# Kernel optimization log

Measured on AMD Instinct MI355X. Metric: run time of the kernel, lower is better.

## Reference

```python
import jax, jax.numpy as jnp
import numpy as np

K_MASK = -2.3819763e+38
NUM_HEADS = 16
NUM_KV_HEADS = 8
HEAD_DIM = 128
FEATURES = 2048
QUERY_SCALE = 0.08838834764831845  # head_dim ** -0.5
ROPE_BASE = 10000
SOFT_CAP = 50.0
WINDOW = 1024


def apply_rope(inputs, positions, base_frequency=ROPE_BASE):
    # inputs: [B, L, N, H], positions: [B, L]
    head_dim = inputs.shape[-1]
    fraction = 2.0 * jnp.arange(0, head_dim // 2, dtype=jnp.float32) / head_dim
    timescale = jnp.asarray(base_frequency, jnp.float32) ** fraction
    sinusoid = positions[..., None].astype(jnp.float32) / timescale[None, None, :]
    sinusoid = sinusoid[..., None, :]  # [B, L, 1, H/2]
    sin, cos = jnp.sin(sinusoid), jnp.cos(sinusoid)
    first, second = jnp.split(inputs, 2, axis=-1)
    out = jnp.concatenate([first * cos - second * sin,
                           second * cos + first * sin], axis=-1)
    return out.astype(inputs.dtype)


def setup_inputs() -> dict:
    key = jax.random.key(0)
    ks = jax.random.split(key, 4)
    B, T, D = 2, 2048, FEATURES
    x = jax.random.normal(ks[0], (B, T, D), dtype=jnp.float32)
    segment_pos = jnp.broadcast_to(jnp.arange(T, dtype=jnp.int32)[None, :], (B, T))
    # causal prefill mask [B, T, S] with S == T
    attn_mask = jnp.broadcast_to(
        jnp.tril(jnp.ones((T, T), dtype=bool))[None], (B, T, T))
    wq = jax.random.normal(ks[1], (NUM_HEADS, D, HEAD_DIM), dtype=jnp.float32) * 0.02
    wkv = jax.random.normal(ks[2], (2, NUM_KV_HEADS, D, HEAD_DIM), dtype=jnp.float32) * 0.02
    wo = jax.random.normal(ks[3], (NUM_HEADS, HEAD_DIM, D), dtype=jnp.float32) * 0.02
    return {"x": x, "segment_pos": segment_pos, "attn_mask": attn_mask,
            "wq": wq, "wkv": wkv, "wo": wo}


def reference(x, segment_pos, attn_mask, wq, wkv, wo):
    # Projections
    q = jnp.einsum('BTD,NDH->BTNH', x, wq)              # [B,T,N,H]
    kv = jnp.einsum('BSD,CKDH->CBSKH', x, wkv)          # [2,B,S,K,H]
    k, v = kv[0], kv[1]

    # RoPE + query scaling
    q = apply_rope(q, segment_pos) * QUERY_SCALE
    k = apply_rope(k, segment_pos)

    # GQA: fold query heads into (K groups, G heads per group)
    B, T, N, H = q.shape
    K, G = NUM_KV_HEADS, N // NUM_KV_HEADS
    qg = q.reshape(B, T, K, G, H)
    logits = jnp.einsum('BTKGH,BSKH->BTKGS', qg, k).reshape(B, T, N, -1)

    # Logit soft-capping
    logits = jnp.tanh(logits / SOFT_CAP) * SOFT_CAP

    # Sliding-window mask (prefill: end_index=0, cache_len = S)
    S = attn_mask.shape[-1]
    cache_positions = jnp.arange(S)[None, None, :]       # [1,1,S]
    sp = segment_pos[:, :, None]                         # [B,T,1]
    sliding = (cache_positions > sp - WINDOW) & (cache_positions < sp + WINDOW)
    mask = jnp.logical_and(attn_mask, sliding)

    padded = jnp.where(mask[:, :, None, :], logits, K_MASK)
    probs = jax.nn.softmax(padded, axis=-1).astype(k.dtype)

    pg = probs.reshape(B, T, K, G, S)
    encoded = jnp.einsum('BTKGS,BSKH->BTKGH', pg, v).reshape(B, T, N, H)
    return jnp.einsum('BTNH,NHD->BTD', encoded, wo)
```

## Files before the change

kernel.cpp:

```cpp
#include <hip/hip_runtime.h>

typedef __attribute__((ext_vector_type(8))) short short8;
typedef __attribute__((ext_vector_type(4))) float f32x4;
typedef __attribute__((ext_vector_type(4))) float f4;
typedef __attribute__((ext_vector_type(4))) unsigned short u16x4;

#define MFMA_B16 __builtin_amdgcn_mfma_f32_16x16x32_bf16

__device__ __forceinline__ unsigned short f2bf(float f) {
    union { float f; unsigned int u; } v; v.f = f;
    unsigned int r = v.u + 0x7fffu + ((v.u >> 16) & 1u);
    return (unsigned short)(r >> 16);
}
__device__ __forceinline__ float bf2f(unsigned short h) {
    union { unsigned int u; float f; } v; v.u = ((unsigned int)h) << 16;
    return v.f;
}
__device__ __forceinline__ float fexp2(float x) {
    float r; asm("v_exp_f32 %0, %1" : "=v"(r) : "v"(x)); return r;
}
__device__ __forceinline__ unsigned int cvt_pk_bf16(float lo, float hi) {
    unsigned int r;
    asm("v_cvt_pk_bf16_f32 %0, %1, %2" : "=v"(r) : "v"(lo), "v"(hi));
    return r;
}
__device__ __forceinline__ void gload_lds16(const void* g, void* l) {
    __builtin_amdgcn_global_load_lds(
        (const __attribute__((address_space(1))) unsigned int*)g,
        (__attribute__((address_space(3))) unsigned int*)l, 16, 0, 0);
}


__global__ void conv_x(const float* __restrict__ x, unsigned short* __restrict__ xb) {
    int i = blockIdx.x * 256 + threadIdx.x;
    f4 v = ((const f4*)x)[i];
    u16x4 o;
    o[0] = f2bf(v[0]); o[1] = f2bf(v[1]); o[2] = f2bf(v[2]); o[3] = f2bf(v[3]);
    ((u16x4*)xb)[i] = o;
}

__global__ void conv_wqkvt(const float* __restrict__ wq, const float* __restrict__ wkv,
                           unsigned short* __restrict__ wt) {
    __shared__ float tile[64 * 65];
    const int d0 = blockIdx.x * 64, f0 = blockIdx.y * 64;
    const int head = f0 >> 7;
    const int h0 = f0 & 127;
    const float* src;
    float scl;
    if (head < 16)      { src = wq + (size_t)head * 2048 * 128;         scl = 0.08838834764831845f; }
    else if (head < 24) { src = wkv + (size_t)(head - 16) * 2048 * 128; scl = 0.057707801635558534f; }
    else                { src = wkv + (size_t)(head - 16) * 2048 * 128; scl = 1.f; }
    {
        int hh = threadIdx.x & 63, dq = threadIdx.x >> 6;
        #pragma unroll
        for (int r = 0; r < 16; ++r) {
            int dd = r * 4 + dq;
            tile[dd * 65 + hh] = src[(size_t)(d0 + dd) * 128 + h0 + hh] * scl;
        }
    }
    __syncthreads();
    {
        int dd = threadIdx.x & 63, fq = threadIdx.x >> 6;
        #pragma unroll
        for (int r = 0; r < 16; ++r) {
            int fl = r * 4 + fq;
            wt[(size_t)(f0 + fl) * 2048 + d0 + dd] = f2bf(tile[dd * 65 + fl]);
        }
    }
}

__global__ void conv_wot(const float* __restrict__ wo, unsigned short* __restrict__ wt) {
    __shared__ float tile[64 * 65];
    const int d0 = blockIdx.x * 64, r0 = blockIdx.y * 64;
    int cc = threadIdx.x & 63, rq = threadIdx.x >> 6;
    #pragma unroll
    for (int r = 0; r < 16; ++r) {
        int rr = r * 4 + rq;
        tile[rr * 65 + cc] = wo[(size_t)(r0 + rr) * 2048 + d0 + cc];
    }
    __syncthreads();
    #pragma unroll
    for (int r = 0; r < 16; ++r) {
        int rr = r * 4 + rq;
        wt[(size_t)(d0 + rr) * 2048 + r0 + cc] = f2bf(tile[cc * 65 + rr]);
    }
}


__global__ __launch_bounds__(512, 2)
void gemm8p(const unsigned short* __restrict__ A,
            const unsigned short* __restrict__ Bt,
            unsigned short* __restrict__ C,
            int ldk, int ldc, int nt, int ksplit, size_t cstride) {
    __shared__ __align__(16) unsigned short LDS[65536];
    const int tid = threadIdx.x, lane = tid & 63, w = tid >> 6;
    const int wr = w >> 2, wc = w & 3;
    const int l15 = lane & 15, l4 = lane >> 4;
    int nwg = gridDim.x * gridDim.y;
    int wg = blockIdx.y * gridDim.x + blockIdx.x;
    int swz = (wg & 7) * (nwg >> 3) + (wg >> 3);
    int bx = swz % gridDim.x, by = swz / gridDim.x;
    int slice = 0;
    if (ksplit) { slice = by & 1; by >>= 1; }
    unsigned short* Cs = C + (size_t)slice * cstride;
    const int brow = by * 256, bcol = bx * 256;
    const size_t koff = (size_t)slice * nt * 64;
    const int wg_a = w & 3;
    const int wg_b = wr;
    const int rA = wg_a * 8 + (lane >> 3);
    const int rB = wg_b * 8 + (lane >> 3);
    const int cgS = ((lane & 7) ^ (lane >> 3)) * 8;
    const unsigned short* aP = A + (size_t)(brow + wr * 128 + rA) * ldk + koff + cgS;
    const unsigned short* bP = Bt + (size_t)(bcol + wc * 64 + rB) * ldk + koff + cgS;
    const int ldsA0 = wr * 8192 + (wg_a * 64 + lane) * 8;
    const int ldsB0 = wc * 4096 + (wg_b * 64 + lane) * 8;
    const int aRd = (wr * 128 + l15) * 64;
    const int bRd = (wc * 64 + l15) * 64;
    const int c0 = ((0 + l4) ^ (l15 & 7)) * 8;
    const int c1 = ((4 + l4) ^ (l15 & 7)) * 8;
    f32x4 acc[8][4] = {};
    gload_lds16(aP,                    &LDS[ldsA0]);
    gload_lds16(bP,                    &LDS[16384 + ldsB0]);
    gload_lds16(aP + (size_t)32 * ldk, &LDS[ldsA0 + 2048]);
    gload_lds16(bP + (size_t)16 * ldk, &LDS[16384 + ldsB0 + 1024]);
    gload_lds16(bP + (size_t)32 * ldk, &LDS[16384 + ldsB0 + 2048]);
    gload_lds16(bP + (size_t)48 * ldk, &LDS[16384 + ldsB0 + 3072]);
    gload_lds16(aP + (size_t)64 * ldk, &LDS[ldsA0 + 4096]);
    gload_lds16(aP + (size_t)96 * ldk, &LDS[ldsA0 + 6144]);
    {
        const unsigned short* a1 = aP + 64;
        const unsigned short* b1 = bP + 64;
        gload_lds16(a1,                    &LDS[32768 + ldsA0]);
        gload_lds16(b1,                    &LDS[49152 + ldsB0]);
        gload_lds16(a1 + (size_t)32 * ldk, &LDS[32768 + ldsA0 + 2048]);
        gload_lds16(b1 + (size_t)16 * ldk, &LDS[49152 + ldsB0 + 1024]);
        gload_lds16(b1 + (size_t)32 * ldk, &LDS[49152 + ldsB0 + 2048]);
        gload_lds16(b1 + (size_t)48 * ldk, &LDS[49152 + ldsB0 + 3072]);
    }
    asm volatile("s_waitcnt vmcnt(6)" ::: "memory");
    __builtin_amdgcn_s_barrier();
    __builtin_amdgcn_sched_barrier(0);

    short8 af[4][2], bl[2][2], bh[2][2];
    for (int t = 0; t < nt - 1; ++t) {
        const int bufA = (t & 1) << 15, bufB = bufA + 16384;
        const int sA = ((t + 1) & 1) << 15;
        const bool pf2 = (t + 2) < nt;
        const unsigned short* ap1 = aP + (size_t)(t + 1) * 64;
        const unsigned short* ap2 = aP + (size_t)(t + 2) * 64;
        const unsigned short* bp2 = bP + (size_t)(t + 2) * 64;
        #pragma unroll
        for (int m = 0; m < 4; ++m) {
            af[m][0] = *(const short8*)&LDS[bufA + aRd + m * 1024 + c0];
            af[m][1] = *(const short8*)&LDS[bufA + aRd + m * 1024 + c1];
        }
        #pragma unroll
        for (int n = 0; n < 2; ++n) {
            bl[n][0] = *(const short8*)&LDS[bufB + bRd + n * 1024 + c0];
            bl[n][1] = *(const short8*)&LDS[bufB + bRd + n * 1024 + c1];
        }
        gload_lds16(ap1 + (size_t)64 * ldk, &LDS[sA + ldsA0 + 4096]);
        gload_lds16(ap1 + (size_t)96 * ldk, &LDS[sA + ldsA0 + 6144]);
        __builtin_amdgcn_s_barrier();
        __builtin_amdgcn_sched_barrier(0);
        __builtin_amdgcn_s_setprio(1);
        #pragma unroll
        for (int kk = 0; kk < 2; ++kk)
            #pragma unroll
            for (int m = 0; m < 4; ++m)
                #pragma unroll
                for (int n = 0; n < 2; ++n)
                    acc[m][n] = MFMA_B16(af[m][kk], bl[n][kk], acc[m][n], 0, 0, 0);
        __builtin_amdgcn_s_setprio(0);
        asm volatile("s_waitcnt vmcnt(6)" ::: "memory");
        __builtin_amdgcn_s_barrier();
        __builtin_amdgcn_sched_barrier(0);
        #pragma unroll
        for (int n = 0; n < 2; ++n) {
            bh[n][0] = *(const short8*)&LDS[bufB + bRd + (n + 2) * 1024 + c0];
            bh[n][1] = *(const short8*)&LDS[bufB + bRd + (n + 2) * 1024 + c1];
        }
        if (pf2) { gload_lds16(ap2, &LDS[bufA + ldsA0]);
                   gload_lds16(bp2, &LDS[bufB + ldsB0]); }
        __builtin_amdgcn_s_barrier();
        __builtin_amdgcn_sched_barrier(0);
        __builtin_amdgcn_s_setprio(1);
        #pragma unroll
        for (int kk = 0; kk < 2; ++kk)
            #pragma unroll
            for (int m = 0; m < 4; ++m)
                #pragma unroll
                for (int n = 0; n < 2; ++n)
                    acc[m][n + 2] = MFMA_B16(af[m][kk], bh[n][kk], acc[m][n + 2], 0, 0, 0);
        __builtin_amdgcn_s_setprio(0);
        asm volatile("s_waitcnt vmcnt(6)" ::: "memory");
        __builtin_amdgcn_s_barrier();
        __builtin_amdgcn_sched_barrier(0);
        #pragma unroll
        for (int m = 0; m < 4; ++m) {
            af[m][0] = *(const short8*)&LDS[bufA + aRd + (m + 4) * 1024 + c0];
            af[m][1] = *(const short8*)&LDS[bufA + aRd + (m + 4) * 1024 + c1];
        }
        if (pf2) { gload_lds16(ap2 + (size_t)32 * ldk, &LDS[bufA + ldsA0 + 2048]);
                   gload_lds16(bp2 + (size_t)16 * ldk, &LDS[bufB + ldsB0 + 1024]); }
        __builtin_amdgcn_s_barrier();
        __builtin_amdgcn_sched_barrier(0);
        __builtin_amdgcn_s_setprio(1);
        #pragma unroll
        for (int kk = 0; kk < 2; ++kk)
            #pragma unroll
            for (int m = 0; m < 4; ++m)
                #pragma unroll
                for (int n = 0; n < 2; ++n)
                    acc[m + 4][n] = MFMA_B16(af[m][kk], bl[n][kk], acc[m + 4][n], 0, 0, 0);
        __builtin_amdgcn_s_setprio(0);
        asm volatile("s_waitcnt vmcnt(6)" ::: "memory");
        __builtin_amdgcn_s_barrier();
        __builtin_amdgcn_sched_barrier(0);
        if (pf2) { gload_lds16(bp2 + (size_t)32 * ldk, &LDS[bufB + ldsB0 + 2048]);
                   gload_lds16(bp2 + (size_t)48 * ldk, &LDS[bufB + ldsB0 + 3072]); }
        __builtin_amdgcn_s_barrier();
        __builtin_amdgcn_sched_barrier(0);
        __builtin_amdgcn_s_setprio(1);
        #pragma unroll
        for (int kk = 0; kk < 2; ++kk)
            #pragma unroll
            for (int m = 0; m < 4; ++m)
                #pragma unroll
                for (int n = 0; n < 2; ++n)
                    acc[m + 4][n + 2] = MFMA_B16(af[m][kk], bh[n][kk], acc[m + 4][n + 2], 0, 0, 0);
        __builtin_amdgcn_s_setprio(0);
        asm volatile("s_waitcnt vmcnt(6)" ::: "memory");
        __builtin_amdgcn_s_barrier();
        __builtin_amdgcn_sched_barrier(0);
    }
    asm volatile("s_waitcnt vmcnt(0)" ::: "memory");
    __builtin_amdgcn_s_barrier();
    {
        const int bufA = ((nt - 1) & 1) << 15, bufB = bufA + 16384;
        #pragma unroll
        for (int m = 0; m < 4; ++m) {
            af[m][0] = *(const short8*)&LDS[bufA + aRd + m * 1024 + c0];
            af[m][1] = *(const short8*)&LDS[bufA + aRd + m * 1024 + c1];
        }
        #pragma unroll
        for (int n = 0; n < 2; ++n) {
            bl[n][0] = *(const short8*)&LDS[bufB + bRd + n * 1024 + c0];
            bl[n][1] = *(const short8*)&LDS[bufB + bRd + n * 1024 + c1];
            bh[n][0] = *(const short8*)&LDS[bufB + bRd + (n + 2) * 1024 + c0];
            bh[n][1] = *(const short8*)&LDS[bufB + bRd + (n + 2) * 1024 + c1];
        }
        #pragma unroll
        for (int kk = 0; kk < 2; ++kk)
            #pragma unroll
            for (int m = 0; m < 4; ++m)
                #pragma unroll
                for (int n = 0; n < 2; ++n) {
                    acc[m][n]     = MFMA_B16(af[m][kk], bl[n][kk], acc[m][n], 0, 0, 0);
                    acc[m][n + 2] = MFMA_B16(af[m][kk], bh[n][kk], acc[m][n + 2], 0, 0, 0);
                }
        #pragma unroll
        for (int m = 0; m < 4; ++m) {
            af[m][0] = *(const short8*)&LDS[bufA + aRd + (m + 4) * 1024 + c0];
            af[m][1] = *(const short8*)&LDS[bufA + aRd + (m + 4) * 1024 + c1];
        }
        #pragma unroll
        for (int kk = 0; kk < 2; ++kk)
            #pragma unroll
            for (int m = 0; m < 4; ++m)
                #pragma unroll
                for (int n = 0; n < 2; ++n) {
                    acc[m + 4][n]     = MFMA_B16(af[m][kk], bl[n][kk], acc[m + 4][n], 0, 0, 0);
                    acc[m + 4][n + 2] = MFMA_B16(af[m][kk], bh[n][kk], acc[m + 4][n + 2], 0, 0, 0);
                }
    }
    #pragma unroll
    for (int m = 0; m < 8; ++m)
        #pragma unroll
        for (int n = 0; n < 4; ++n)
            #pragma unroll
            for (int j = 0; j < 4; ++j) {
                int row = brow + wr * 128 + m * 16 + l4 * 4 + j;
                int col = bcol + wc * 64 + n * 16 + l15;
                Cs[(size_t)row * ldc + col] = f2bf(acc[m][n][j]);
            }
}

__global__ void addparts(const unsigned short* __restrict__ p0,
                         const unsigned short* __restrict__ p1,
                         float* __restrict__ out) {
    int i = blockIdx.x * 256 + threadIdx.x;
    short8 a = ((const short8*)p0)[i];
    short8 b = ((const short8*)p1)[i];
    f4 lo, hi;
    #pragma unroll
    for (int j = 0; j < 4; ++j)
        lo[j] = bf2f((unsigned short)a[j]) + bf2f((unsigned short)b[j]);
    #pragma unroll
    for (int j = 0; j < 4; ++j)
        hi[j] = bf2f((unsigned short)a[j + 4]) + bf2f((unsigned short)b[j + 4]);
    ((f4*)out)[2 * i] = lo;
    ((f4*)out)[2 * i + 1] = hi;
}

__global__ void rope_reshape(const unsigned short* __restrict__ qkv,
                             const int* __restrict__ segpos,
                             unsigned short* __restrict__ q_r,
                             unsigned short* __restrict__ k_r) {
    const int bt = blockIdx.x;
    const int hd = blockIdx.y * 2 + (threadIdx.x >> 7);
    const int b = bt >> 11, t = bt & 2047;
    const int h = threadIdx.x & 127;
    const unsigned short* in = (hd < 16)
        ? qkv + (size_t)bt * 4096 + hd * 128
        : qkv + (size_t)bt * 4096 + 2048 + (hd - 16) * 128;
    int pos = segpos[bt];
    int i = h & 63;
    float inv_ts = __expf((float)i * (-9.210340371976184f / 64.f));
    float ang = (float)pos * inv_ts;
    float s = __sinf(ang), c = __cosf(ang);
    float x1 = bf2f(in[i]);
    float x2 = bf2f(in[i + 64]);
    float o = (h < 64) ? (x1 * c - x2 * s) : (x2 * c + x1 * s);
    if (hd < 16) {
        q_r[((size_t)((b * 16 + hd) * 2048 + t)) * 128 + h] = f2bf(o);
    } else {
        int kh = hd - 16;
        k_r[((size_t)((b * 8 + kh) * 2048 + t)) * 128 + h] = f2bf(o);
    }
}

__global__ void v_transpose(const unsigned short* __restrict__ qkv,
                            unsigned short* __restrict__ v_t) {
    __shared__ unsigned short tile[64][72];
    const int tt0 = blockIdx.x * 64;
    const int kh = blockIdx.y >> 1, hb = (blockIdx.y & 1) * 64;
    const int b = blockIdx.z;
    int c = threadIdx.x & 63, rq = threadIdx.x >> 6;
    #pragma unroll
    for (int r = 0; r < 16; ++r) {
        int tt = r * 4 + rq;
        tile[tt][c] = qkv[(size_t)(b * 2048 + tt0 + tt) * 4096 + 3072 + kh * 128 + hb + c];
    }
    __syncthreads();
    #pragma unroll
    for (int r = 0; r < 16; ++r) {
        int hr = r * 4 + rq;
        v_t[((size_t)(b * 8 + kh) * 128 + hb + hr) * 2048 + tt0 + c] = tile[c][hr];
    }
}


__device__ __forceinline__ void stage_kv(const unsigned short* kbase, const unsigned short* vbase,
                                         unsigned short* Ksb, unsigned short* Vtb,
                                         int st, int tid) {
    #pragma unroll
    for (int r = 0; r < 2; ++r) {
        int e = (r * 512 + tid) * 8;
        int krow = e >> 7, kcol = e & 127;
        gload_lds16(kbase + (size_t)(st * 64 + krow) * 128 + (kcol ^ ((krow & 7) << 3)), Ksb + e);
        int vrow = e >> 6, vcol = e & 63;
        gload_lds16(vbase + (size_t)vrow * 2048 + st * 64 + (vcol ^ ((vrow & 7) << 3)), Vtb + e);
    }
}

__global__ __launch_bounds__(512, 4)
void attn_kernel(const unsigned short* __restrict__ q_r,
                 const unsigned short* __restrict__ k_r,
                 const unsigned short* __restrict__ v_t,
                 unsigned short* __restrict__ enc) {
    __shared__ __align__(16) unsigned short Ks[2][64 * 128];
    __shared__ __align__(16) unsigned short Vt[2][128 * 64];
    __shared__ __align__(16) unsigned short Pl[8][16 * 64];
    const int tid = threadIdx.x, lane = tid & 63, wave = tid >> 6;
    const int l15 = lane & 15, l4 = lane >> 4;
    const int flat = blockIdx.x;
    const int xcd = flat & 7, g = flat >> 3;
    const int pair = xcd * 2 + (g >> 5);
    const int qb = 31 - (g & 31);
    const int kh = pair >> 1, b = pair & 1;
    const int n = kh * 2 + (wave >> 2);
    const int wq = wave & 3;
    short8 qf[4];
    {
        const unsigned short* qp =
            q_r + ((size_t)((b * 16 + n) * 2048 + qb * 64 + wq * 16 + l15)) * 128 + l4 * 8;
        #pragma unroll
        for (int kk = 0; kk < 4; ++kk) qf[kk] = *(const short8*)(qp + kk * 32);
    }
    f32x4 Of[8] = {};
    float lrow[4] = {};
    int t_lo = qb * 64 - 1023; if (t_lo < 0) t_lo = 0;
    const int st0 = t_lo >> 6;
    const unsigned short* kbase = k_r + (size_t)(b * 8 + kh) * 2048 * 128;
    const unsigned short* vbase = v_t + (size_t)(b * 8 + kh) * 128 * 2048;

    stage_kv(kbase, vbase, Ks[0], Vt[0], st0, tid);
    __syncthreads();
    int cur = 0;
    for (int st = st0; st <= qb; ++st) {
        if (st < qb)
            stage_kv(kbase, vbase, Ks[cur ^ 1], Vt[cur ^ 1], st + 1, tid);
        f32x4 sf[4] = {};
        __builtin_amdgcn_s_setprio(1);
        #pragma unroll
        for (int nc = 0; nc < 4; ++nc) {
            int row = nc * 16 + l15;
            int sw = (l15 & 7) << 3;
            #pragma unroll
            for (int kk = 0; kk < 4; ++kk) {
                short8 bfr = *(const short8*)&Ks[cur][row * 128 + ((kk * 32 + l4 * 8) ^ sw)];
                sf[nc] = MFMA_B16(qf[kk], bfr, sf[nc], 0, 0, 0);
            }
        }
        __builtin_amdgcn_s_setprio(0);
        const int mode = (st == qb) ? 1 : ((qb >= 16 && st == st0) ? 2 : 0);
        #pragma unroll
        for (int j = 0; j < 4; ++j) {
            int trow = qb * 64 + wq * 16 + l4 * 4 + j;
            int prow = l4 * 4 + j;
            int psw = (prow & 7) << 3;
            float pp[4];
            #pragma unroll
            for (int nc = 0; nc < 4; ++nc) {
                float ex = fexp2(sf[nc][j]);
                float p = fexp2(-144.26950408889634f * __builtin_amdgcn_rcpf(ex + 1.f));
                if (mode) {
                    int s = st * 64 + nc * 16 + l15;
                    bool ok = (mode == 1) ? (s <= trow) : (s >= trow - 1023);
                    p = ok ? p : 0.f;
                }
                lrow[j] += p;
                pp[nc] = p;
            }
            unsigned int k01 = cvt_pk_bf16(pp[0], pp[1]);
            unsigned int k23 = cvt_pk_bf16(pp[2], pp[3]);
            unsigned short* Pr = &Pl[wave][prow * 64];
            Pr[l15 ^ psw]        = (unsigned short)k01;
            Pr[(16 + l15) ^ psw] = (unsigned short)(k01 >> 16);
            Pr[(32 + l15) ^ psw] = (unsigned short)k23;
            Pr[(48 + l15) ^ psw] = (unsigned short)(k23 >> 16);
        }
        {
            int asw = (l15 & 7) << 3;
            __builtin_amdgcn_s_setprio(1);
            #pragma unroll
            for (int ks = 0; ks < 2; ++ks) {
                short8 af = *(const short8*)&Pl[wave][l15 * 64 + ((ks * 32 + l4 * 8) ^ asw)];
                #pragma unroll
                for (int hc = 0; hc < 8; ++hc) {
                    int vrow = hc * 16 + l15;
                    short8 bfr = *(const short8*)&Vt[cur][vrow * 64 + ((ks * 32 + l4 * 8) ^ asw)];
                    Of[hc] = MFMA_B16(af, bfr, Of[hc], 0, 0, 0);
                }
            }
            __builtin_amdgcn_s_setprio(0);
        }
        __syncthreads();
        cur ^= 1;
    }
    float inv[4];
    #pragma unroll
    for (int j = 0; j < 4; ++j) {
        float l = lrow[j];
        l += __shfl_xor(l, 1); l += __shfl_xor(l, 2);
        l += __shfl_xor(l, 4); l += __shfl_xor(l, 8);
        inv[j] = 1.f / l;
    }
    #pragma unroll
    for (int hc = 0; hc < 8; ++hc)
        #pragma unroll
        for (int j = 0; j < 4; ++j) {
            size_t row = (size_t)(b * 2048 + qb * 64 + wq * 16 + l4 * 4 + j);
            enc[row * 2048 + n * 128 + hc * 16 + l15] = f2bf(Of[hc][j] * inv[j]);
        }
}


extern "C" void kernel_launch(void* const* d_in, const int* in_sizes, int n_in,
                              void* d_out, int out_size, void* d_ws, size_t ws_size,
                              hipStream_t stream) {
    const float* x   = (const float*)d_in[0];
    const int* segp  = (const int*)d_in[1];
    const float* wq  = (const float*)d_in[3];
    const float* wkv = (const float*)d_in[4];
    const float* wo  = (const float*)d_in[5];
    float* out = (float*)d_out;
    char* ws = (char*)d_ws;
    if (ws_size < ((size_t)96 << 20)) return;

    unsigned short* xb    = (unsigned short*)(ws);
    unsigned short* wqkvt = (unsigned short*)(ws + ((size_t)16 << 20));
    unsigned short* qkv   = (unsigned short*)(ws + ((size_t)32 << 20));
    unsigned short* q_r   = (unsigned short*)(ws + ((size_t)64 << 20));
    unsigned short* k_r   = (unsigned short*)(ws + ((size_t)80 << 20));
    unsigned short* v_t   = (unsigned short*)(ws + ((size_t)88 << 20));
    unsigned short* wo_t  = (unsigned short*)(ws + ((size_t)16 << 20));
    unsigned short* enc   = (unsigned short*)(ws + ((size_t)32 << 20));
    unsigned short* part  = (unsigned short*)(ws + ((size_t)64 << 20));

    conv_x<<<8192, 256, 0, stream>>>(x, xb);
    conv_wqkvt<<<dim3(32, 64), 256, 0, stream>>>(wq, wkv, wqkvt);
    gemm8p<<<dim3(16, 16), 512, 0, stream>>>(xb, wqkvt, qkv, 2048, 4096, 32, 0, 0);
    rope_reshape<<<dim3(4096, 12), 256, 0, stream>>>(qkv, segp, q_r, k_r);
    v_transpose<<<dim3(32, 16, 2), 256, 0, stream>>>(qkv, v_t);
    conv_wot<<<dim3(32, 32), 256, 0, stream>>>(wo, wo_t);
    attn_kernel<<<512, 512, 0, stream>>>(q_r, k_r, v_t, enc);
    gemm8p<<<dim3(8, 32), 512, 0, stream>>>(enc, wo_t, part, 2048, 2048, 16, 1, (size_t)4096 * 2048);
    addparts<<<4096, 256, 0, stream>>>(part, part + (size_t)4096 * 2048, out);
}
```

Before: 212.4 us.

## Double query tile per attention block and compute row sums via MFMA

The attention kernel now handles 128 query rows per block (32 per wave) instead of 64, so each staged K/V tile is reused by twice as many queries, and the grid is halved to 256 blocks. Row sums of the probabilities are computed with an extra MFMA against a vector of ones instead of scalar adds plus cross-lane shuffles. The cost is roughly double the register use and a lower occupancy bound of 2, fewer blocks to spread across CUs, and a masking mode that now has to cover two diagonal tiles.

```diff
diff --git a/kernel.cpp b/kernel.cpp
--- a/kernel.cpp
+++ b/kernel.cpp
@@ -364,44 +364,49 @@
     }
 }
 
-__global__ __launch_bounds__(512, 4)
+__global__ __launch_bounds__(512, 2)
 void attn_kernel(const unsigned short* __restrict__ q_r,
                  const unsigned short* __restrict__ k_r,
                  const unsigned short* __restrict__ v_t,
                  unsigned short* __restrict__ enc) {
     __shared__ __align__(16) unsigned short Ks[2][64 * 128];
     __shared__ __align__(16) unsigned short Vt[2][128 * 64];
-    __shared__ __align__(16) unsigned short Pl[8][16 * 64];
+    __shared__ __align__(16) unsigned short Pl[8][32 * 64];
     const int tid = threadIdx.x, lane = tid & 63, wave = tid >> 6;
     const int l15 = lane & 15, l4 = lane >> 4;
     const int flat = blockIdx.x;
     const int xcd = flat & 7, g = flat >> 3;
-    const int pair = xcd * 2 + (g >> 5);
-    const int qb = 31 - (g & 31);
+    const int pair = xcd * 2 + (g >> 4);
+    const int qb = 15 - (g & 15);
     const int kh = pair >> 1, b = pair & 1;
     const int n = kh * 2 + (wave >> 2);
     const int wq = wave & 3;
-    short8 qf[4];
-    {
+    short8 qf[2][4];
+    #pragma unroll
+    for (int r = 0; r < 2; ++r) {
         const unsigned short* qp =
-            q_r + ((size_t)((b * 16 + n) * 2048 + qb * 64 + wq * 16 + l15)) * 128 + l4 * 8;
-        #pragma unroll
-        for (int kk = 0; kk < 4; ++kk) qf[kk] = *(const short8*)(qp + kk * 32);
-    }
-    f32x4 Of[8] = {};
-    float lrow[4] = {};
-    int t_lo = qb * 64 - 1023; if (t_lo < 0) t_lo = 0;
+            q_r + ((size_t)((b * 16 + n) * 2048 + qb * 128 + wq * 32 + r * 16 + l15)) * 128 + l4 * 8;
+        #pragma unroll
+        for (int kk = 0; kk < 4; ++kk) qf[r][kk] = *(const short8*)(qp + kk * 32);
+    }
+    short8 ones;
+    #pragma unroll
+    for (int e = 0; e < 8; ++e) ones[e] = (short)0x3F80;
+    f32x4 Of[2][8] = {};
+    f32x4 accl[2] = {};
+    int t_lo = qb * 128 - 1023; if (t_lo < 0) t_lo = 0;
     const int st0 = t_lo >> 6;
+    const int stL = qb * 2 + 1;
     const unsigned short* kbase = k_r + (size_t)(b * 8 + kh) * 2048 * 128;
     const unsigned short* vbase = v_t + (size_t)(b * 8 + kh) * 128 * 2048;
 
     stage_kv(kbase, vbase, Ks[0], Vt[0], st0, tid);
     __syncthreads();
     int cur = 0;
-    for (int st = st0; st <= qb; ++st) {
-        if (st < qb)
+    for (int st = st0; st <= stL; ++st) {
+        if (st < stL)
             stage_kv(kbase, vbase, Ks[cur ^ 1], Vt[cur ^ 1], st + 1, tid);
-        f32x4 sf[4] = {};
+        f32x4 sf[2][4] = {};
         __builtin_amdgcn_s_setprio(1);
         #pragma unroll
         for (int nc = 0; nc < 4; ++nc) {
@@ -410,70 +415,76 @@
             #pragma unroll
             for (int kk = 0; kk < 4; ++kk) {
                 short8 bfr = *(const short8*)&Ks[cur][row * 128 + ((kk * 32 + l4 * 8) ^ sw)];
-                sf[nc] = MFMA_B16(qf[kk], bfr, sf[nc], 0, 0, 0);
+                sf[0][nc] = MFMA_B16(qf[0][kk], bfr, sf[0][nc], 0, 0, 0);
+                sf[1][nc] = MFMA_B16(qf[1][kk], bfr, sf[1][nc], 0, 0, 0);
             }
         }
         __builtin_amdgcn_s_setprio(0);
-        const int mode = (st == qb) ? 1 : ((qb >= 16 && st == st0) ? 2 : 0);
-        #pragma unroll
-        for (int j = 0; j < 4; ++j) {
-            int trow = qb * 64 + wq * 16 + l4 * 4 + j;
-            int prow = l4 * 4 + j;
-            int psw = (prow & 7) << 3;
-            float pp[4];
-            #pragma unroll
-            for (int nc = 0; nc < 4; ++nc) {
-                float ex = fexp2(sf[nc][j]);
-                float p = fexp2(-144.26950408889634f * __builtin_amdgcn_rcpf(ex + 1.f));
-                if (mode) {
-                    int s = st * 64 + nc * 16 + l15;
-                    bool ok = (mode == 1) ? (s <= trow) : (s >= trow - 1023);
-                    p = ok ? p : 0.f;
+        const int mode = ((st >= 2 * qb) ? 1 : 0) | ((qb >= 8 && st <= st0 + 1) ? 2 : 0);
+        #pragma unroll
+        for (int r = 0; r < 2; ++r) {
+            #pragma unroll
+            for (int j = 0; j < 4; ++j) {
+                int trow = qb * 128 + wq * 32 + r * 16 + l4 * 4 + j;
+                int prow = r * 16 + l4 * 4 + j;
+                int psw = (prow & 7) << 3;
+                float pp[4];
+                #pragma unroll
+                for (int nc = 0; nc < 4; ++nc) {
+                    float ex = fexp2(sf[r][nc][j]);
+                    float p = fexp2(-144.26950408889634f * __builtin_amdgcn_rcpf(ex + 1.f));
+                    if (mode) {
+                        int s = st * 64 + nc * 16 + l15;
+                        bool ok = true;
+                        if (mode & 1) ok = ok && (s <= trow);
+                        if (mode & 2) ok = ok && (s >= trow - 1023);
+                        p = ok ? p : 0.f;
+                    }
+                    pp[nc] = p;
                 }
-                lrow[j] += p;
-                pp[nc] = p;
+                unsigned int k01 = cvt_pk_bf16(pp[0], pp[1]);
+                unsigned int k23 = cvt_pk_bf16(pp[2], pp[3]);
+                unsigned short* Pr = &Pl[wave][prow * 64];
+                Pr[l15 ^ psw]        = (unsigned short)k01;
+                Pr[(16 + l15) ^ psw] = (unsigned short)(k01 >> 16);
+                Pr[(32 + l15) ^ psw] = (unsigned short)k23;
+                Pr[(48 + l15) ^ psw] = (unsigned short)(k23 >> 16);
             }
-            unsigned int k01 = cvt_pk_bf16(pp[0], pp[1]);
-            unsigned int k23 = cvt_pk_bf16(pp[2], pp[3]);
-            unsigned short* Pr = &Pl[wave][prow * 64];
-            Pr[l15 ^ psw]        = (unsigned short)k01;
-            Pr[(16 + l15) ^ psw] = (unsigned short)(k01 >> 16);
-            Pr[(32 + l15) ^ psw] = (unsigned short)k23;
-            Pr[(48 + l15) ^ psw] = (unsigned short)(k23 >> 16);
         }
         {
             int asw = (l15 & 7) << 3;
             __builtin_amdgcn_s_setprio(1);
             #pragma unroll
-            for (int ks = 0; ks < 2; ++ks) {
-                short8 af = *(const short8*)&Pl[wave][l15 * 64 + ((ks * 32 + l4 * 8) ^ asw)];
-                #pragma unroll
-                for (int hc = 0; hc < 8; ++hc) {
-                    int vrow = hc * 16 + l15;
-                    short8 bfr = *(const short8*)&Vt[cur][vrow * 64 + ((ks * 32 + l4 * 8) ^ asw)];
-                    Of[hc] = MFMA_B16(af, bfr, Of[hc], 0, 0, 0);
+            for (int rr = 0; rr < 2; ++rr)
+                #pragma unroll
+                for (int ks = 0; ks < 2; ++ks) {
+                    short8 af = *(const short8*)&Pl[wave][(rr * 16 + l15) * 64 + ((ks * 32 + l4 * 8) ^ asw)];
+                    accl[rr] = MFMA_B16(af, ones, accl[rr], 0, 0, 0);
+                    #pragma unroll
+                    for (int hc = 0; hc < 8; ++hc) {
+                        int vrow = hc * 16 + l15;
+                        short8 bfr = *(const short8*)&Vt[cur][vrow * 64 + ((ks * 32 + l4 * 8) ^ asw)];
+                        Of[rr][hc] = MFMA_B16(af, bfr, Of[rr][hc], 0, 0, 0);
+                    }
                 }
-            }
             __builtin_amdgcn_s_setprio(0);
         }
         __syncthreads();
         cur ^= 1;
     }
-    float inv[4];
-    #pragma unroll
-    for (int j = 0; j < 4; ++j) {
-        float l = lrow[j];
-        l += __shfl_xor(l, 1); l += __shfl_xor(l, 2);
-        l += __shfl_xor(l, 4); l += __shfl_xor(l, 8);
-        inv[j] = 1.f / l;
-    }
-    #pragma unroll
-    for (int hc = 0; hc < 8; ++hc)
-        #pragma unroll
-        for (int j = 0; j < 4; ++j) {
-            size_t row = (size_t)(b * 2048 + qb * 64 + wq * 16 + l4 * 4 + j);
-            enc[row * 2048 + n * 128 + hc * 16 + l15] = f2bf(Of[hc][j] * inv[j]);
-        }
+    #pragma unroll
+    for (int rr = 0; rr < 2; ++rr) {
+        f32x4 inv;
+        #pragma unroll
+        for (int j = 0; j < 4; ++j) inv[j] = 1.f / accl[rr][j];
+        #pragma unroll
+        for (int hc = 0; hc < 8; ++hc)
+            #pragma unroll
+            for (int j = 0; j < 4; ++j) {
+                size_t row = (size_t)(b * 2048 + qb * 128 + wq * 32 + rr * 16 + l4 * 4 + j);
+                enc[row * 2048 + n * 128 + hc * 16 + l15] = f2bf(Of[rr][hc][j] * inv[j]);
+            }
+    }
 }
 
 
@@ -505,7 +516,7 @@
     rope_reshape<<<dim3(4096, 12), 256, 0, stream>>>(qkv, segp, q_r, k_r);
     v_transpose<<<dim3(32, 16, 2), 256, 0, stream>>>(qkv, v_t);
     conv_wot<<<dim3(32, 32), 256, 0, stream>>>(wo, wo_t);
-    attn_kernel<<<512, 512, 0, stream>>>(q_r, k_r, v_t, enc);
+    attn_kernel<<<256, 512, 0, stream>>>(q_r, k_r, v_t, enc);
     gemm8p<<<dim3(8, 32), 512, 0, stream>>>(enc, wo_t, part, 2048, 2048, 16, 1, (size_t)4096 * 2048);
     addparts<<<4096, 256, 0, stream>>>(part, part + (size_t)4096 * 2048, out);
 }
```

New measurement: 218.1 us. 1.03x slower.
